# Kernel optimization log

Hardware: AMD Instinct MI355X
Metric: run time of the kernel (lower is better)

## Reference

```python
import jax, jax.numpy as jnp
import numpy as np

IN, OUT, IO, CF, CS = 128, 128, 512, 512, 1024
B = 8192
TAU_IO, TAU_CF, TAU_CS = 2.0, 5.0, 70.0


def _lin(x, W, b):
    # torch nn.Linear: y = x @ W.T + b, W has shape [out, in]
    return x @ W.T + b


def setup_inputs() -> dict:
    key = jax.random.key(0)
    ks = jax.random.split(key, 24)

    def wb(i, fan_out, fan_in):
        s = 1.0 / np.sqrt(fan_in)
        W = jax.random.uniform(ks[2 * i], (fan_out, fan_in), jnp.float32, -s, s)
        b = jax.random.uniform(ks[2 * i + 1], (fan_out,), jnp.float32, -s, s)
        return W, b

    Wi2io, bi2io = wb(0, IO, IN)
    Wio2o, bio2o = wb(1, OUT, IO)
    Wio2io, bio2io = wb(2, IO, IO)
    Wio2cf, bio2cf = wb(3, CF, IO)
    Wcf2io, bcf2io = wb(4, IO, CF)
    Wcf2cs, bcf2cs = wb(5, CS, CF)
    Wcf2cf, bcf2cf = wb(6, CF, CF)
    Wcs2cf, bcs2cf = wb(7, CF, CS)
    Wcs2cs, bcs2cs = wb(8, CS, CS)

    x = jax.random.normal(ks[18], (B, IN), jnp.float32)
    io_state = jnp.zeros((B, IO), jnp.float32)
    cf_state = jnp.zeros((B, CF), jnp.float32)
    cs_state = jnp.zeros((B, CS), jnp.float32)

    return dict(
        x=x, io_state=io_state, cf_state=cf_state, cs_state=cs_state,
        Wi2io=Wi2io, bi2io=bi2io, Wio2o=Wio2o, bio2o=bio2o,
        Wio2io=Wio2io, bio2io=bio2io, Wio2cf=Wio2cf, bio2cf=bio2cf,
        Wcf2io=Wcf2io, bcf2io=bcf2io, Wcf2cs=Wcf2cs, bcf2cs=bcf2cs,
        Wcf2cf=Wcf2cf, bcf2cf=bcf2cf, Wcs2cf=Wcs2cf, bcs2cf=bcs2cf,
        Wcs2cs=Wcs2cs, bcs2cs=bcs2cs,
    )


def reference(x, io_state, cf_state, cs_state,
              Wi2io, bi2io, Wio2o, bio2o,
              Wio2io, bio2io, Wio2cf, bio2cf,
              Wcf2io, bcf2io, Wcf2cs, bcf2cs,
              Wcf2cf, bcf2cf, Wcs2cf, bcs2cf,
              Wcs2cs, bcs2cs):
    x = x.reshape(-1, IN)
    # leaky-integrated updates; all branches read the *previous* states
    io_new = jnp.tanh(
        (1.0 - 1.0 / TAU_IO) * io_state
        + (_lin(io_state, Wio2io, bio2io)
           + _lin(cf_state, Wcf2io, bcf2io)
           + _lin(x, Wi2io, bi2io)) / TAU_IO)
    cf_new = jnp.tanh(
        (1.0 - 1.0 / TAU_CF) * cf_state
        + (_lin(cf_state, Wcf2cf, bcf2cf)
           + _lin(cs_state, Wcs2cf, bcs2cf)
           + _lin(io_state, Wio2cf, bio2cf)) / TAU_CF)
    cs_new = jnp.tanh(
        (1.0 - 1.0 / TAU_CS) * cs_state
        + (_lin(cs_state, Wcs2cs, bcs2cs)
           + _lin(cf_state, Wcf2cs, bcf2cs)) / TAU_CS)
    y = jnp.tanh(_lin(io_new, Wio2o, bio2o))
    return y
```

## Files before the change

kernel.cpp:

```cpp
#include <hip/hip_runtime.h>


typedef float f32x4 __attribute__((ext_vector_type(4)));
typedef __bf16 bf16x4 __attribute__((ext_vector_type(4)));
typedef __bf16 bf16x8 __attribute__((ext_vector_type(8)));
typedef unsigned short u16x4 __attribute__((ext_vector_type(4)));

__device__ __forceinline__ unsigned short f2bf(float f) {
    unsigned u = __builtin_bit_cast(unsigned, f);
    u += 0x7FFFu + ((u >> 16) & 1u);
    return (unsigned short)(u >> 16);
}

__device__ __forceinline__ float tanh_fast(float x) {
    float e = __expf(2.0f * x);
    return 1.0f - 2.0f * __builtin_amdgcn_rcpf(e + 1.0f);
}

__device__ __forceinline__ void gload16(const void* g, void* l) {
    __builtin_amdgcn_global_load_lds(
        (const __attribute__((address_space(1))) void*)g,
        (__attribute__((address_space(3))) void*)l, 16, 0, 0);
}

__device__ __forceinline__ void wait_barrier() {
    asm volatile("s_waitcnt vmcnt(0)\n\ts_barrier" ::: "memory");
}

__global__ __launch_bounds__(256) void k_convert(
    const float* __restrict__ Wi2io, const float* __restrict__ Wio2io,
    const float* __restrict__ Wcf2io, const float* __restrict__ Wio2o,
    const float* __restrict__ b1, const float* __restrict__ b2,
    const float* __restrict__ b3,
    unsigned short* __restrict__ wcat, unsigned short* __restrict__ w2s,
    float* __restrict__ bsum)
{
    int idx = blockIdx.x * 256 + threadIdx.x;
    if (idx < 147456) {
        int n = idx / 288;
        int k = (idx - n * 288) * 4;
        const float* s;
        if (k < 128)      s = Wi2io  + n * 128 + k;
        else if (k < 640) s = Wio2io + n * 512 + (k - 128);
        else              s = Wcf2io + n * 512 + (k - 640);
        f32x4 v = *(const f32x4*)s;
        u16x4 h;
        #pragma unroll
        for (int t = 0; t < 4; ++t) {
            float f = 0.5f * v[t];
            int kk = k + t;
            if (kk >= 128 && kk < 640 && (kk - 128) == n) f += 0.5f;
            h[t] = f2bf(f);
        }
        int ad = n * 1152 + (k & ~63) + ((((k >> 3) & 7) ^ (n & 7)) << 3) + (k & 7);
        *(u16x4*)(wcat + ad) = h;
    } else if (idx < 163840) {
        int q = idx - 147456;
        int n = q >> 7;
        int k = (q & 127) * 4;
        f32x4 v = *(const f32x4*)(Wio2o + n * 512 + k);
        u16x4 h; h[0]=f2bf(v[0]); h[1]=f2bf(v[1]); h[2]=f2bf(v[2]); h[3]=f2bf(v[3]);
        int ad = n * 512 + (k & ~63) + ((((k >> 3) & 7) ^ (n & 7)) << 3) + (k & 7);
        *(u16x4*)(w2s + ad) = h;
    } else if (idx < 164352) {
        int n = idx - 163840;
        bsum[n] = 0.5f * (b1[n] + b2[n] + b3[n]);
    }
}

__global__ __launch_bounds__(256, 2) void k_gemm1(
    const float* __restrict__ x, const float* __restrict__ io,
    const float* __restrict__ cf,
    const unsigned short* __restrict__ wcat,
    const float* __restrict__ bsum,
    unsigned short* __restrict__ ionew)
{
    __shared__ __align__(16) char lds[2][32768];

    const int tid = threadIdx.x, b = blockIdx.x;
    const int xcd = b & 7, idx = b >> 3;
    const int m0 = ((xcd << 4) | (idx & 15)) << 6;
    const int n0 = (idx >> 4) << 7;

    const int lane = tid & 63, wid = tid >> 6;
    const int li = lane & 15, lh = lane >> 4;
    const int wm = (wid >> 1) << 5;
    const int wn = (wid & 1) << 6;

    int a_off_x[4], a_off_s[4], b_off[4];
    #pragma unroll
    for (int j = 0; j < 4; ++j) {
        int r = (wid << 4) + 4 * j + (lane >> 4);
        int cs = (li ^ (r & 15)) << 2;
        a_off_x[j] = (m0 + r) * 128 + cs;
        a_off_s[j] = (m0 + r) * 512 + cs;
        int rb = (wid << 5) + 8 * j + (lane >> 3);
        b_off[j] = (n0 + rb) * 1152 + ((lane & 7) << 3);
    }
    const int adst = wid << 12;

    f32x4 zz = {0.f, 0.f, 0.f, 0.f};
    f32x4 acc[2][4];
    #pragma unroll
    for (int i = 0; i < 2; ++i)
        #pragma unroll
        for (int j = 0; j < 4; ++j) acc[i][j] = zz;

#define STAGE1(KT, BUF) do {                                                   \
        int K_ = (KT);                                                         \
        char* A_ = (BUF); char* B_ = (BUF) + 16384;                            \
        if (K_ < 2) {                                                          \
            const float* sp = x + (K_ << 6);                                   \
            _Pragma("unroll")                                                  \
            for (int j = 0; j < 4; ++j)                                        \
                gload16(sp + a_off_x[j], A_ + adst + j * 1024);                \
        } else if (K_ < 10) {                                                  \
            const float* sp = io + ((K_ - 2) << 6);                            \
            _Pragma("unroll")                                                  \
            for (int j = 0; j < 4; ++j)                                        \
                gload16(sp + a_off_s[j], A_ + adst + j * 1024);                \
        } else {                                                               \
            const float* sp = cf + ((K_ - 10) << 6);                           \
            _Pragma("unroll")                                                  \
            for (int j = 0; j < 4; ++j)                                        \
                gload16(sp + a_off_s[j], A_ + adst + j * 1024);                \
        }                                                                      \
        const unsigned short* wp = wcat + (K_ << 6);                           \
        _Pragma("unroll")                                                      \
        for (int j = 0; j < 4; ++j)                                            \
            gload16(wp + b_off[j], B_ + adst + j * 1024);                      \
    } while (0)

#define COMPUTE1(BUF) do {                                                     \
        const char* A_ = (BUF); const char* B_ = (BUF) + 16384;                \
        _Pragma("unroll")                                                      \
        for (int ks = 0; ks < 2; ++ks) {                                       \
            bf16x8 af[2];                                                      \
            _Pragma("unroll")                                                  \
            for (int mi = 0; mi < 2; ++mi) {                                   \
                int r = wm + mi * 16 + li;                                     \
                int c0 = ks * 8 + lh * 2;                                      \
                f32x4 a0 = *(const f32x4*)(A_ + r * 256 +                      \
                                           ((c0 ^ (r & 15)) << 4));            \
                f32x4 a1 = *(const f32x4*)(A_ + r * 256 +                      \
                                           (((c0 + 1) ^ (r & 15)) << 4));      \
                bf16x4 h0 = __builtin_convertvector(a0, bf16x4);               \
                bf16x4 h1 = __builtin_convertvector(a1, bf16x4);               \
                af[mi] = __builtin_shufflevector(h0, h1, 0,1,2,3,4,5,6,7);     \
            }                                                                  \
            _Pragma("unroll")                                                  \
            for (int nj = 0; nj < 4; ++nj) {                                   \
                int rb = wn + nj * 16 + li;                                    \
                int cb = ks * 4 + lh;                                          \
                bf16x8 bv = *(const bf16x8*)(B_ + rb * 128 +                   \
                                             ((cb ^ (rb & 7)) << 4));          \
                acc[0][nj] = __builtin_amdgcn_mfma_f32_16x16x32_bf16(          \
                    af[0], bv, acc[0][nj], 0, 0, 0);                           \
                acc[1][nj] = __builtin_amdgcn_mfma_f32_16x16x32_bf16(          \
                    af[1], bv, acc[1][nj], 0, 0, 0);                           \
            }                                                                  \
        }                                                                      \
    } while (0)

    STAGE1(0, lds[0]);
    wait_barrier();
    #pragma unroll 1
    for (int kt = 0; kt < 18; ++kt) {
        if (kt + 1 < 18) STAGE1(kt + 1, lds[(kt + 1) & 1]);
        COMPUTE1(lds[kt & 1]);
        wait_barrier();
    }
#undef STAGE1
#undef COMPUTE1

    #pragma unroll
    for (int nj = 0; nj < 4; ++nj) {
        int gn = n0 + wn + nj * 16 + li;
        float bb = bsum[gn];
        #pragma unroll
        for (int mi = 0; mi < 2; ++mi) {
            #pragma unroll
            for (int r = 0; r < 4; ++r) {
                int gm = m0 + wm + mi * 16 + (lh << 2) + r;
                float v = tanh_fast(acc[mi][nj][r] + bb);
                int ad = gm * 512 + (gn & ~63) +
                         ((((gn >> 3) & 7) ^ (gm & 7)) << 3) + (gn & 7);
                ionew[ad] = f2bf(v);
            }
        }
    }
}

__global__ __launch_bounds__(256, 2) void k_gemm2(
    const unsigned short* __restrict__ ionew,
    const unsigned short* __restrict__ w2s,
    const float* __restrict__ b4,
    float* __restrict__ out)
{
    __shared__ __align__(16) char lds[2][20480];

    const int tid = threadIdx.x, b = blockIdx.x;
    const int xcd = b & 7, idx = b >> 3;
    const int m0 = ((xcd << 5) | idx) << 5;

    const int lane = tid & 63, wid = tid >> 6;
    const int li = lane & 15, lh = lane >> 4;
    const int wn = wid << 5;

    const int a2_off = (m0 + (wid << 3) + (lane >> 3)) * 512 + ((lane & 7) << 3);
    int b2_off[4];
    #pragma unroll
    for (int j = 0; j < 4; ++j)
        b2_off[j] = ((wid << 5) + 8 * j + (lane >> 3)) * 512 + ((lane & 7) << 3);

    f32x4 zz = {0.f, 0.f, 0.f, 0.f};
    f32x4 acc[2][2];
    acc[0][0] = zz; acc[0][1] = zz; acc[1][0] = zz; acc[1][1] = zz;

#define STAGE2(KT, BUF) do {                                                   \
        int K_ = (KT);                                                         \
        char* A_ = (BUF); char* B_ = (BUF) + 4096;                             \
        gload16(ionew + a2_off + (K_ << 6), A_ + (wid << 10));                 \
        _Pragma("unroll")                                                      \
        for (int j = 0; j < 4; ++j)                                            \
            gload16(w2s + b2_off[j] + (K_ << 6), B_ + (wid << 12) + j * 1024); \
    } while (0)

#define COMPUTE2(BUF) do {                                                     \
        const char* A_ = (BUF); const char* B_ = (BUF) + 4096;                 \
        _Pragma("unroll")                                                      \
        for (int ks = 0; ks < 2; ++ks) {                                       \
            int c = ks * 4 + lh;                                               \
            bf16x8 av[2];                                                      \
            _Pragma("unroll")                                                  \
            for (int mi = 0; mi < 2; ++mi) {                                   \
                int r = mi * 16 + li;                                          \
                av[mi] = *(const bf16x8*)(A_ + r * 128 + ((c ^ (r & 7)) << 4));\
            }                                                                  \
            _Pragma("unroll")                                                  \
            for (int nj = 0; nj < 2; ++nj) {                                   \
                int rb = wn + nj * 16 + li;                                    \
                bf16x8 bv = *(const bf16x8*)(B_ + rb * 128 +                   \
                                             ((c ^ (rb & 7)) << 4));           \
                acc[0][nj] = __builtin_amdgcn_mfma_f32_16x16x32_bf16(          \
                    av[0], bv, acc[0][nj], 0, 0, 0);                           \
                acc[1][nj] = __builtin_amdgcn_mfma_f32_16x16x32_bf16(          \
                    av[1], bv, acc[1][nj], 0, 0, 0);                           \
            }                                                                  \
        }                                                                      \
    } while (0)

    STAGE2(0, lds[0]);
    wait_barrier();
    #pragma unroll 1
    for (int kt = 0; kt < 8; ++kt) {
        if (kt + 1 < 8) STAGE2(kt + 1, lds[(kt + 1) & 1]);
        COMPUTE2(lds[kt & 1]);
        wait_barrier();
    }
#undef STAGE2
#undef COMPUTE2

    #pragma unroll
    for (int nj = 0; nj < 2; ++nj) {
        int n = wn + nj * 16 + li;
        float bb = b4[n];
        #pragma unroll
        for (int mi = 0; mi < 2; ++mi) {
            #pragma unroll
            for (int r = 0; r < 4; ++r) {
                int gm = m0 + mi * 16 + (lh << 2) + r;
                out[(size_t)gm * 128 + n] = tanh_fast(acc[mi][nj][r] + bb);
            }
        }
    }
}

extern "C" void kernel_launch(void* const* d_in, const int* in_sizes, int n_in,
                              void* d_out, int out_size, void* d_ws, size_t ws_size,
                              hipStream_t stream)
{
    const float* x      = (const float*)d_in[0];
    const float* io     = (const float*)d_in[1];
    const float* cf     = (const float*)d_in[2];
    const float* Wi2io  = (const float*)d_in[4];
    const float* bi2io  = (const float*)d_in[5];
    const float* Wio2o  = (const float*)d_in[6];
    const float* bio2o  = (const float*)d_in[7];
    const float* Wio2io = (const float*)d_in[8];
    const float* bio2io = (const float*)d_in[9];
    const float* Wcf2io = (const float*)d_in[12];
    const float* bcf2io = (const float*)d_in[13];
    float* out = (float*)d_out;

    char* ws = (char*)d_ws;
    unsigned short* wcat  = (unsigned short*)ws;
    unsigned short* w2s   = (unsigned short*)(ws + 1179648);
    float*          bsum  = (float*)(ws + 1310720);
    unsigned short* ionew = (unsigned short*)(ws + 1312768);

    hipLaunchKernelGGL(k_convert, dim3(642), dim3(256), 0, stream,
                       Wi2io, Wio2io, Wcf2io, Wio2o, bi2io, bio2io, bcf2io,
                       wcat, w2s, bsum);
    hipLaunchKernelGGL(k_gemm1, dim3(512), dim3(256), 0, stream,
                       x, io, cf, wcat, bsum, ionew);
    hipLaunchKernelGGL(k_gemm2, dim3(256), dim3(256), 0, stream,
                       ionew, w2s, bio2o, out);
}
```

Before: 34.62 us.

## Fuse both GEMMs into one kernel keeping io_new tile in LDS

Merges the two GEMM kernels into one 512-thread kernel per 32-row tile that computes the full 512-wide io_new row block. It keeps the result as bf16 in LDS and immediately runs the output projection. This removes the global round-trip of the intermediate io_new and one kernel launch. The loads also switch to a deeper two-stage prefetch with partial vmcnt waits. In exchange it uses about 144KB of LDS per block at one block per CU and launches only 256 blocks, which lowers occupancy, and each block rereads the full weight matrix.

```diff
diff --git a/kernel.cpp b/kernel.cpp
--- a/kernel.cpp
+++ b/kernel.cpp
@@ -23,9 +23,8 @@
         (__attribute__((address_space(3))) void*)l, 16, 0, 0);
 }
 
-__device__ __forceinline__ void wait_barrier() {
-    asm volatile("s_waitcnt vmcnt(0)\n\ts_barrier" ::: "memory");
-}
+#define WAITB(N) asm volatile("s_waitcnt vmcnt(" #N ") lgkmcnt(0)\n\ts_barrier" ::: "memory")
+#define BARL()   asm volatile("s_waitcnt lgkmcnt(0)\n\ts_barrier" ::: "memory")
 
 __global__ __launch_bounds__(256) void k_convert(
     const float* __restrict__ Wi2io, const float* __restrict__ Wio2io,
@@ -68,36 +67,35 @@
     }
 }
 
-__global__ __launch_bounds__(256, 2) void k_gemm1(
+__global__ __launch_bounds__(512) void k_fused(
     const float* __restrict__ x, const float* __restrict__ io,
     const float* __restrict__ cf,
     const unsigned short* __restrict__ wcat,
-    const float* __restrict__ bsum,
-    unsigned short* __restrict__ ionew)
+    const unsigned short* __restrict__ w2s,
+    const float* __restrict__ bsum, const float* __restrict__ b4,
+    float* __restrict__ out)
 {
-    __shared__ __align__(16) char lds[2][32768];
-
-    const int tid = threadIdx.x, b = blockIdx.x;
-    const int xcd = b & 7, idx = b >> 3;
-    const int m0 = ((xcd << 4) | (idx & 15)) << 6;
-    const int n0 = (idx >> 4) << 7;
-
+    __shared__ __align__(16) char lds[147456];
+
+    const int tid = threadIdx.x;
+    const int m0  = blockIdx.x << 5;
     const int lane = tid & 63, wid = tid >> 6;
     const int li = lane & 15, lh = lane >> 4;
-    const int wm = (wid >> 1) << 5;
-    const int wn = (wid & 1) << 6;
-
-    int a_off_x[4], a_off_s[4], b_off[4];
+
+    const int arow = (wid << 2) + (lane >> 4);
+    const int acs  = (lane & 15) ^ (arow & 15);
+    const size_t a_x = (size_t)(m0 + arow) * 128 + acs * 4;
+    const size_t a_s = (size_t)(m0 + arow) * 512 + acs * 4;
+    int b_src[8];
     #pragma unroll
-    for (int j = 0; j < 4; ++j) {
-        int r = (wid << 4) + 4 * j + (lane >> 4);
-        int cs = (li ^ (r & 15)) << 2;
-        a_off_x[j] = (m0 + r) * 128 + cs;
-        a_off_s[j] = (m0 + r) * 512 + cs;
-        int rb = (wid << 5) + 8 * j + (lane >> 3);
-        b_off[j] = (n0 + rb) * 1152 + ((lane & 7) << 3);
-    }
-    const int adst = wid << 12;
+    for (int j = 0; j < 8; ++j) {
+        int rb = (wid << 6) + (j << 3) + (lane >> 3);
+        b_src[j] = rb * 1152 + ((lane & 7) << 3);
+    }
+    int w_src[2];
+    #pragma unroll
+    for (int j = 0; j < 2; ++j)
+        w_src[j] = ((wid << 4) + (j << 3) + (lane >> 3)) * 512 + ((lane & 7) << 3);
 
     f32x4 zz = {0.f, 0.f, 0.f, 0.f};
     f32x4 acc[2][4];
@@ -106,40 +104,31 @@
         #pragma unroll
         for (int j = 0; j < 4; ++j) acc[i][j] = zz;
 
-#define STAGE1(KT, BUF) do {                                                   \
+#define STAGE1(KT, BASE) do {                                                  \
         int K_ = (KT);                                                         \
-        char* A_ = (BUF); char* B_ = (BUF) + 16384;                            \
-        if (K_ < 2) {                                                          \
-            const float* sp = x + (K_ << 6);                                   \
-            _Pragma("unroll")                                                  \
-            for (int j = 0; j < 4; ++j)                                        \
-                gload16(sp + a_off_x[j], A_ + adst + j * 1024);                \
-        } else if (K_ < 10) {                                                  \
-            const float* sp = io + ((K_ - 2) << 6);                            \
-            _Pragma("unroll")                                                  \
-            for (int j = 0; j < 4; ++j)                                        \
-                gload16(sp + a_off_s[j], A_ + adst + j * 1024);                \
-        } else {                                                               \
-            const float* sp = cf + ((K_ - 10) << 6);                           \
-            _Pragma("unroll")                                                  \
-            for (int j = 0; j < 4; ++j)                                        \
-                gload16(sp + a_off_s[j], A_ + adst + j * 1024);                \
-        }                                                                      \
+        if (K_ < 2)       gload16(x  + (K_ << 6) + a_x,                        \
+                                  lds + (BASE) + (wid << 10));                 \
+        else if (K_ < 10) gload16(io + ((K_ - 2) << 6) + a_s,                  \
+                                  lds + (BASE) + (wid << 10));                 \
+        else              gload16(cf + ((K_ - 10) << 6) + a_s,                 \
+                                  lds + (BASE) + (wid << 10));                 \
         const unsigned short* wp = wcat + (K_ << 6);                           \
         _Pragma("unroll")                                                      \
-        for (int j = 0; j < 4; ++j)                                            \
-            gload16(wp + b_off[j], B_ + adst + j * 1024);                      \
-    } while (0)
-
-#define COMPUTE1(BUF) do {                                                     \
-        const char* A_ = (BUF); const char* B_ = (BUF) + 16384;                \
+        for (int j = 0; j < 8; ++j)                                            \
+            gload16(wp + b_src[j],                                             \
+                    lds + (BASE) + 8192 + (wid << 13) + (j << 10));            \
+    } while (0)
+
+#define COMPUTE1(BASE) do {                                                    \
+        const char* A_ = lds + (BASE);                                         \
+        const char* Bb = lds + (BASE) + 8192;                                  \
         _Pragma("unroll")                                                      \
         for (int ks = 0; ks < 2; ++ks) {                                       \
+            int c0 = ks * 8 + lh * 2;                                          \
             bf16x8 af[2];                                                      \
             _Pragma("unroll")                                                  \
             for (int mi = 0; mi < 2; ++mi) {                                   \
-                int r = wm + mi * 16 + li;                                     \
-                int c0 = ks * 8 + lh * 2;                                      \
+                int r = mi * 16 + li;                                          \
                 f32x4 a0 = *(const f32x4*)(A_ + r * 256 +                      \
                                            ((c0 ^ (r & 15)) << 4));            \
                 f32x4 a1 = *(const f32x4*)(A_ + r * 256 +                      \
@@ -148,12 +137,12 @@
                 bf16x4 h1 = __builtin_convertvector(a1, bf16x4);               \
                 af[mi] = __builtin_shufflevector(h0, h1, 0,1,2,3,4,5,6,7);     \
             }                                                                  \
+            int c = ks * 4 + lh;                                               \
             _Pragma("unroll")                                                  \
             for (int nj = 0; nj < 4; ++nj) {                                   \
-                int rb = wn + nj * 16 + li;                                    \
-                int cb = ks * 4 + lh;                                          \
-                bf16x8 bv = *(const bf16x8*)(B_ + rb * 128 +                   \
-                                             ((cb ^ (rb & 7)) << 4));          \
+                int rb = (wid << 6) + nj * 16 + li;                            \
+                bf16x8 bv = *(const bf16x8*)(Bb + rb * 128 +                   \
+                                             ((c ^ (rb & 7)) << 4));           \
                 acc[0][nj] = __builtin_amdgcn_mfma_f32_16x16x32_bf16(          \
                     af[0], bv, acc[0][nj], 0, 0, 0);                           \
                 acc[1][nj] = __builtin_amdgcn_mfma_f32_16x16x32_bf16(          \
@@ -162,118 +151,98 @@
         }                                                                      \
     } while (0)
 
-    STAGE1(0, lds[0]);
-    wait_barrier();
+#define W2STAGE(KT, WBASE) do {                                                \
+        const unsigned short* wp2 = w2s + ((KT) << 6);                         \
+        gload16(wp2 + w_src[0], lds + (WBASE) + (wid << 11));                  \
+        gload16(wp2 + w_src[1], lds + (WBASE) + (wid << 11) + 1024);           \
+    } while (0)
+
+    STAGE1(0, 0);
+    STAGE1(1, 73728);
     #pragma unroll 1
-    for (int kt = 0; kt < 18; ++kt) {
-        if (kt + 1 < 18) STAGE1(kt + 1, lds[(kt + 1) & 1]);
-        COMPUTE1(lds[kt & 1]);
-        wait_barrier();
-    }
-#undef STAGE1
-#undef COMPUTE1
-
-    #pragma unroll
-    for (int nj = 0; nj < 4; ++nj) {
-        int gn = n0 + wn + nj * 16 + li;
-        float bb = bsum[gn];
+    for (int t = 0; t < 17; ++t) {
+        WAITB(9);
+        int cb = (t & 1) ? 73728 : 0;
+        COMPUTE1(cb);
+        BARL();
+        if (t + 2 < 18) STAGE1(t + 2, cb);
+    }
+    WAITB(0);
+    W2STAGE(0, 36864);
+    W2STAGE(1, 53248);
+    COMPUTE1(73728);
+
+    {
+        unsigned short* IO16 = (unsigned short*)lds;
+        #pragma unroll
+        for (int nj = 0; nj < 4; ++nj) {
+            int gn = (wid << 6) + nj * 16 + li;
+            float bb = bsum[gn];
+            #pragma unroll
+            for (int mi = 0; mi < 2; ++mi) {
+                #pragma unroll
+                for (int r = 0; r < 4; ++r) {
+                    int m = mi * 16 + (lh << 2) + r;
+                    float v = tanh_fast(acc[mi][nj][r] + bb);
+                    int ad = m * 512 + (gn & ~63) +
+                             ((((gn >> 3) & 7) ^ (m & 7)) << 3) + (gn & 7);
+                    IO16[ad] = f2bf(v);
+                }
+            }
+        }
+    }
+
+    f32x4 acc2[2];
+    acc2[0] = zz; acc2[1] = zz;
+
+#define COMPUTE2(KT, WBASE) do {                                               \
+        _Pragma("unroll")                                                      \
+        for (int ks = 0; ks < 2; ++ks) {                                       \
+            int c = ks * 4 + lh;                                               \
+            bf16x8 af2[2];                                                     \
+            _Pragma("unroll")                                                  \
+            for (int mi = 0; mi < 2; ++mi) {                                   \
+                int m = mi * 16 + li;                                          \
+                af2[mi] = *(const bf16x8*)(lds + m * 1024 + ((KT) << 7) +      \
+                                           ((c ^ (m & 7)) << 4));              \
+            }                                                                  \
+            int rb = (wid << 4) + li;                                          \
+            bf16x8 bv = *(const bf16x8*)(lds + (WBASE) + rb * 128 +            \
+                                         ((c ^ (rb & 7)) << 4));               \
+            acc2[0] = __builtin_amdgcn_mfma_f32_16x16x32_bf16(                 \
+                af2[0], bv, acc2[0], 0, 0, 0);                                 \
+            acc2[1] = __builtin_amdgcn_mfma_f32_16x16x32_bf16(                 \
+                af2[1], bv, acc2[1], 0, 0, 0);                                 \
+        }                                                                      \
+    } while (0)
+
+    #pragma unroll 1
+    for (int t2 = 0; t2 < 7; ++t2) {
+        WAITB(2);
+        int wb = (t2 & 1) ? 53248 : 36864;
+        COMPUTE2(t2, wb);
+        BARL();
+        if (t2 + 2 < 8) W2STAGE(t2 + 2, wb);
+    }
+    WAITB(0);
+    COMPUTE2(7, 53248);
+
+    {
+        int n = (wid << 4) + li;
+        float bb = b4[n];
         #pragma unroll
         for (int mi = 0; mi < 2; ++mi) {
             #pragma unroll
             for (int r = 0; r < 4; ++r) {
-                int gm = m0 + wm + mi * 16 + (lh << 2) + r;
-                float v = tanh_fast(acc[mi][nj][r] + bb);
-                int ad = gm * 512 + (gn & ~63) +
-                         ((((gn >> 3) & 7) ^ (gm & 7)) << 3) + (gn & 7);
-                ionew[ad] = f2bf(v);
+                int m = mi * 16 + (lh << 2) + r;
+                out[(size_t)(m0 + m) * 128 + n] = tanh_fast(acc2[mi][r] + bb);
             }
         }
     }
-}
-
-__global__ __launch_bounds__(256, 2) void k_gemm2(
-    const unsigned short* __restrict__ ionew,
-    const unsigned short* __restrict__ w2s,
-    const float* __restrict__ b4,
-    float* __restrict__ out)
-{
-    __shared__ __align__(16) char lds[2][20480];
-
-    const int tid = threadIdx.x, b = blockIdx.x;
-    const int xcd = b & 7, idx = b >> 3;
-    const int m0 = ((xcd << 5) | idx) << 5;
-
-    const int lane = tid & 63, wid = tid >> 6;
-    const int li = lane & 15, lh = lane >> 4;
-    const int wn = wid << 5;
-
-    const int a2_off = (m0 + (wid << 3) + (lane >> 3)) * 512 + ((lane & 7) << 3);
-    int b2_off[4];
-    #pragma unroll
-    for (int j = 0; j < 4; ++j)
-        b2_off[j] = ((wid << 5) + 8 * j + (lane >> 3)) * 512 + ((lane & 7) << 3);
-
-    f32x4 zz = {0.f, 0.f, 0.f, 0.f};
-    f32x4 acc[2][2];
-    acc[0][0] = zz; acc[0][1] = zz; acc[1][0] = zz; acc[1][1] = zz;
-
-#define STAGE2(KT, BUF) do {                                                   \
-        int K_ = (KT);                                                         \
-        char* A_ = (BUF); char* B_ = (BUF) + 4096;                             \
-        gload16(ionew + a2_off + (K_ << 6), A_ + (wid << 10));                 \
-        _Pragma("unroll")                                                      \
-        for (int j = 0; j < 4; ++j)                                            \
-            gload16(w2s + b2_off[j] + (K_ << 6), B_ + (wid << 12) + j * 1024); \
-    } while (0)
-
-#define COMPUTE2(BUF) do {                                                     \
-        const char* A_ = (BUF); const char* B_ = (BUF) + 4096;                 \
-        _Pragma("unroll")                                                      \
-        for (int ks = 0; ks < 2; ++ks) {                                       \
-            int c = ks * 4 + lh;                                               \
-            bf16x8 av[2];                                                      \
-            _Pragma("unroll")                                                  \
-            for (int mi = 0; mi < 2; ++mi) {                                   \
-                int r = mi * 16 + li;                                          \
-                av[mi] = *(const bf16x8*)(A_ + r * 128 + ((c ^ (r & 7)) << 4));\
-            }                                                                  \
-            _Pragma("unroll")                                                  \
-            for (int nj = 0; nj < 2; ++nj) {                                   \
-                int rb = wn + nj * 16 + li;                                    \
-                bf16x8 bv = *(const bf16x8*)(B_ + rb * 128 +                   \
-                                             ((c ^ (rb & 7)) << 4));           \
-                acc[0][nj] = __builtin_amdgcn_mfma_f32_16x16x32_bf16(          \
-                    av[0], bv, acc[0][nj], 0, 0, 0);                           \
-                acc[1][nj] = __builtin_amdgcn_mfma_f32_16x16x32_bf16(          \
-                    av[1], bv, acc[1][nj], 0, 0, 0);                           \
-            }                                                                  \
-        }                                                                      \
-    } while (0)
-
-    STAGE2(0, lds[0]);
-    wait_barrier();
-    #pragma unroll 1
-    for (int kt = 0; kt < 8; ++kt) {
-        if (kt + 1 < 8) STAGE2(kt + 1, lds[(kt + 1) & 1]);
-        COMPUTE2(lds[kt & 1]);
-        wait_barrier();
-    }
-#undef STAGE2
+#undef STAGE1
+#undef COMPUTE1
+#undef W2STAGE
 #undef COMPUTE2
-
-    #pragma unroll
-    for (int nj = 0; nj < 2; ++nj) {
-        int n = wn + nj * 16 + li;
-        float bb = b4[n];
-        #pragma unroll
-        for (int mi = 0; mi < 2; ++mi) {
-            #pragma unroll
-            for (int r = 0; r < 4; ++r) {
-                int gm = m0 + mi * 16 + (lh << 2) + r;
-                out[(size_t)gm * 128 + n] = tanh_fast(acc[mi][nj][r] + bb);
-            }
-        }
-    }
 }
 
 extern "C" void kernel_launch(void* const* d_in, const int* in_sizes, int n_in,
@@ -294,16 +263,13 @@
     float* out = (float*)d_out;
 
     char* ws = (char*)d_ws;
-    unsigned short* wcat  = (unsigned short*)ws;
-    unsigned short* w2s   = (unsigned short*)(ws + 1179648);
-    float*          bsum  = (float*)(ws + 1310720);
-    unsigned short* ionew = (unsigned short*)(ws + 1312768);
+    unsigned short* wcat = (unsigned short*)ws;
+    unsigned short* w2s  = (unsigned short*)(ws + 1179648);
+    float*          bsum = (float*)(ws + 1310720);
 
     hipLaunchKernelGGL(k_convert, dim3(642), dim3(256), 0, stream,
                        Wi2io, Wio2io, Wcf2io, Wio2o, bi2io, bio2io, bcf2io,
                        wcat, w2s, bsum);
-    hipLaunchKernelGGL(k_gemm1, dim3(512), dim3(256), 0, stream,
-                       x, io, cf, wcat, bsum, ionew);
-    hipLaunchKernelGGL(k_gemm2, dim3(256), dim3(256), 0, stream,
-                       ionew, w2s, bio2o, out);
-}
+    hipLaunchKernelGGL(k_fused, dim3(256), dim3(512), 0, stream,
+                       x, io, cf, wcat, w2s, bsum, bio2o, out);
+}
```

Result: slower. 35.83 us (+3.5%).
